# Performance work log

Measured on AMD Instinct MI355X. Metric: run time of the kernel, lower is better.

Reference implementation:

```python
import jax, jax.numpy as jnp
import numpy as np

N_NODES = 50000
N_EDGES = 1600000
D_NODE = 256
D_EDGE = 64
D_MSG = 256          # out_features_msg; each of node/edge halves is D_MSG // 2
D_OUT = 256          # out_features_reduce
H = D_MSG // 2


def setup_inputs() -> dict:
    key = jax.random.key(0)
    ks = jax.random.split(key, 10)
    x = jax.random.normal(ks[0], (N_NODES, D_NODE), dtype=jnp.float32)
    ez = jax.random.normal(ks[1], (N_EDGES, D_EDGE), dtype=jnp.float32)
    src = jax.random.randint(ks[2], (N_EDGES,), 0, N_NODES, dtype=jnp.int32)
    dst = jax.random.randint(ks[3], (N_EDGES,), 0, N_NODES, dtype=jnp.int32)
    Wn = jax.random.normal(ks[4], (H, D_NODE), dtype=jnp.float32) / np.sqrt(D_NODE)
    bn = jax.random.normal(ks[5], (H,), dtype=jnp.float32) * 0.01
    We = jax.random.normal(ks[6], (H, D_EDGE), dtype=jnp.float32) / np.sqrt(D_EDGE)
    be = jax.random.normal(ks[7], (H,), dtype=jnp.float32) * 0.01
    Wr = jax.random.normal(ks[8], (D_OUT, D_MSG), dtype=jnp.float32) / np.sqrt(D_MSG)
    br = jax.random.normal(ks[9], (D_OUT,), dtype=jnp.float32) * 0.01
    return {"x": x, "ez": ez, "src": src, "dst": dst,
            "Wn": Wn, "bn": bn, "We": We, "be": be, "Wr": Wr, "br": br}


def reference(x, ez, src, dst, Wn, bn, We, be, Wr, br):
    n = x.shape[0]
    # node/edge linear projections (message halves)
    hn = x @ Wn.T + bn                 # [N, H]
    he = ez @ We.T + be                # [E, H]
    # message for edge e is concat(hn[src[e]], he[e]); aggregate sums per dst node.
    sum_n = jax.ops.segment_sum(hn[src], dst, num_segments=n)   # [N, H]
    sum_e = jax.ops.segment_sum(he, dst, num_segments=n)        # [N, H]
    deg = jnp.zeros((n,), dtype=x.dtype).at[dst].add(1.0)       # in-degree
    # local self-state: concat(hn, zeros_H); mean over (deg + 1) states.
    denom = (deg + 1.0)[:, None]
    mean_state = jnp.concatenate([(hn + sum_n) / denom, sum_e / denom], axis=-1)  # [N, D_MSG]
    # reduce_layer is affine, so Linear(mean(states)) == mean(Linear(states)).
    out = mean_state @ Wr.T + br       # [N, D_OUT]
    # DGL degree-bucketing: zero-in-degree nodes get zero-filled output.
    out = jnp.where(deg[:, None] > 0, out, jnp.zeros((), dtype=out.dtype))
    return out
```

## Files before the change

kernel.cpp:

```cpp
#include <hip/hip_runtime.h>

#define N_NODES 50000
#define N_EDGES 1600000
#define D_NODE  256
#define D_EDGE  64
#define H       128
#define D_OUT   256

#define NPAD    50176

typedef __attribute__((ext_vector_type(8))) short bf16x8;
typedef __attribute__((ext_vector_type(4))) float f32x4;
typedef __attribute__((ext_vector_type(4))) unsigned short u16x4;

__device__ __forceinline__ float bf2f(unsigned short u) {
    union { unsigned int i; float f; } v; v.i = ((unsigned int)u) << 16; return v.f;
}
__device__ __forceinline__ unsigned short f2bf(float f) {
    union { float f; unsigned int i; } v; v.f = f;
    unsigned int r = v.i + 0x7FFFu + ((v.i >> 16) & 1u);
    return (unsigned short)(r >> 16);
}

__global__ __launch_bounds__(256) void cvt_kernel(
        const float* __restrict__ Wn, const float* __restrict__ We,
        const float* __restrict__ Wr,
        unsigned short* __restrict__ Wn_b, unsigned short* __restrict__ We_b,
        unsigned short* __restrict__ Wr_b) {
    int b = blockIdx.x;
    const float* s; unsigned short* d; int base;
    if (b < 32)      { s = Wn; d = Wn_b; base = b * 1024; }
    else if (b < 40) { s = We; d = We_b; base = (b - 32) * 1024; }
    else             { s = Wr; d = Wr_b; base = (b - 40) * 1024; }
    int i = base + threadIdx.x * 4;
    f32x4 v = *(const f32x4*)(s + i);
    u16x4 o;
    #pragma unroll
    for (int j = 0; j < 4; ++j) o[j] = f2bf(v[j]);
    *(u16x4*)(d + i) = o;
}

__global__ __launch_bounds__(64) void hn_kernel(
        const float* __restrict__ x,
        const unsigned short* __restrict__ Wn_b,
        const float* __restrict__ bn,
        unsigned short* __restrict__ hn) {
    const int lane = threadIdx.x & 63;
    const int m = lane & 15, q = lane >> 4;
    const int n0 = blockIdx.x * 16;

    f32x4 acc[8];
    #pragma unroll
    for (int t = 0; t < 8; ++t)
        #pragma unroll
        for (int r = 0; r < 4; ++r) acc[t][r] = 0.0f;

    const float* xrow = x + (size_t)(n0 + m) * D_NODE + q * 8;
    #pragma unroll
    for (int kk = 0; kk < 8; ++kk) {
        f32x4 a0 = *(const f32x4*)(xrow + kk * 32);
        f32x4 a1 = *(const f32x4*)(xrow + kk * 32 + 4);
        bf16x8 a;
        #pragma unroll
        for (int j = 0; j < 4; ++j) {
            a[j]     = (short)f2bf(a0[j]);
            a[4 + j] = (short)f2bf(a1[j]);
        }
        #pragma unroll
        for (int t = 0; t < 8; ++t) {
            bf16x8 b = *(const bf16x8*)(Wn_b + (size_t)(t * 16 + m) * D_NODE + kk * 32 + q * 8);
            acc[t] = __builtin_amdgcn_mfma_f32_16x16x32_bf16(a, b, acc[t], 0, 0, 0);
        }
    }
    #pragma unroll
    for (int t = 0; t < 8; ++t) {
        int o = t * 16 + m;
        float bv = bn[o];
        #pragma unroll
        for (int r = 0; r < 4; ++r) {
            int node = n0 + q * 4 + r;
            hn[(size_t)node * H + o] = f2bf(acc[t][r] + bv);
        }
    }
}

__global__ __launch_bounds__(256) void hist_kernel(
        const int* __restrict__ dst, unsigned int* __restrict__ cnt) {
    int e = blockIdx.x * 256 + threadIdx.x;
    atomicAdd(&cnt[dst[e]], 1u);
}

__device__ __forceinline__ unsigned int block_scan_incl(unsigned int v, unsigned int* wtot) {
    const int lane = threadIdx.x & 63;
    const int wid = threadIdx.x >> 6;
    unsigned int x = v;
    #pragma unroll
    for (int off = 1; off < 64; off <<= 1) {
        unsigned int y = __shfl_up(x, off, 64);
        if (lane >= off) x += y;
    }
    if (lane == 63) wtot[wid] = x;
    __syncthreads();
    unsigned int wof = 0;
    #pragma unroll
    for (int w = 0; w < 4; ++w) if (w < wid) wof += wtot[w];
    return x + wof;
}

__global__ __launch_bounds__(256) void scan1_kernel(
        const unsigned int* __restrict__ cnt,
        unsigned int* __restrict__ partial,
        unsigned int* __restrict__ blocksum) {
    __shared__ unsigned int wtot[4];
    int i = blockIdx.x * 256 + threadIdx.x;
    unsigned int v = cnt[i];
    unsigned int inc = block_scan_incl(v, wtot);
    partial[i] = inc - v;
    if (threadIdx.x == 255) blocksum[blockIdx.x] = inc;
}

__global__ __launch_bounds__(256) void scan2_kernel(
        const unsigned int* __restrict__ blocksum,
        unsigned int* __restrict__ blockoff) {
    __shared__ unsigned int wtot[4];
    unsigned int v = blocksum[threadIdx.x];
    unsigned int inc = block_scan_incl(v, wtot);
    blockoff[threadIdx.x] = inc - v;
}

__global__ __launch_bounds__(256) void cursor_kernel(
        const unsigned int* __restrict__ partial,
        const unsigned int* __restrict__ blockoff,
        unsigned int* __restrict__ cursor) {
    int i = blockIdx.x * 256 + threadIdx.x;
    cursor[i] = partial[i] + blockoff[blockIdx.x];
}

__global__ __launch_bounds__(256) void scatter_kernel(
        const int* __restrict__ src, const int* __restrict__ dst,
        unsigned int* __restrict__ cursor,
        unsigned long long* __restrict__ eid_src) {
    int e = blockIdx.x * 256 + threadIdx.x;
    int d = dst[e];
    unsigned int s = (unsigned int)src[e];
    unsigned int pos = atomicAdd(&cursor[d], 1u);
    eid_src[pos] = ((unsigned long long)s << 32) | (unsigned int)e;
}

__global__ __launch_bounds__(256) void agg_kernel(
        const unsigned long long* __restrict__ eid_src,
        const unsigned int* __restrict__ cursor,
        const unsigned int* __restrict__ cnt,
        const float* __restrict__ ez,
        const unsigned int* __restrict__ hn32,
        float* __restrict__ sumN, float* __restrict__ sumEZ) {
    const int n = blockIdx.x * 4 + (threadIdx.x >> 6);
    const int lane = threadIdx.x & 63;
    const unsigned int end = cursor[n];
    const unsigned int c = cnt[n];
    const unsigned int beg = end - c;

    float se = 0.0f, sn0 = 0.0f, sn1 = 0.0f;

    for (unsigned int base = beg; base < end; base += 64) {
        int mcnt = (int)(end - base); if (mcnt > 64) mcnt = 64;
        unsigned long long ent = (lane < mcnt) ? eid_src[base + lane] : 0ULL;
        unsigned int elo = (unsigned int)ent;
        unsigned int shi = (unsigned int)(ent >> 32);

        int j = 0;
        for (; j + 4 <= mcnt; j += 4) {
            unsigned int e0 = __shfl(elo, j, 64),     s0i = __shfl(shi, j, 64);
            unsigned int e1 = __shfl(elo, j + 1, 64), s1i = __shfl(shi, j + 1, 64);
            unsigned int e2 = __shfl(elo, j + 2, 64), s2i = __shfl(shi, j + 2, 64);
            unsigned int e3 = __shfl(elo, j + 3, 64), s3i = __shfl(shi, j + 3, 64);
            float a0 = ez[(size_t)e0 * D_EDGE + lane];
            float a1 = ez[(size_t)e1 * D_EDGE + lane];
            float a2 = ez[(size_t)e2 * D_EDGE + lane];
            float a3 = ez[(size_t)e3 * D_EDGE + lane];
            unsigned int h0 = hn32[(size_t)s0i * 64 + lane];
            unsigned int h1 = hn32[(size_t)s1i * 64 + lane];
            unsigned int h2 = hn32[(size_t)s2i * 64 + lane];
            unsigned int h3 = hn32[(size_t)s3i * 64 + lane];
            se += (a0 + a1) + (a2 + a3);
            union { unsigned int u; float f; } lo, hi;
            lo.u = h0 << 16; hi.u = h0 & 0xffff0000u; sn0 += lo.f; sn1 += hi.f;
            lo.u = h1 << 16; hi.u = h1 & 0xffff0000u; sn0 += lo.f; sn1 += hi.f;
            lo.u = h2 << 16; hi.u = h2 & 0xffff0000u; sn0 += lo.f; sn1 += hi.f;
            lo.u = h3 << 16; hi.u = h3 & 0xffff0000u; sn0 += lo.f; sn1 += hi.f;
        }
        for (; j < mcnt; ++j) {
            unsigned int e0 = __shfl(elo, j, 64), s0i = __shfl(shi, j, 64);
            float a0 = ez[(size_t)e0 * D_EDGE + lane];
            unsigned int h0 = hn32[(size_t)s0i * 64 + lane];
            se += a0;
            union { unsigned int u; float f; } lo, hi;
            lo.u = h0 << 16; hi.u = h0 & 0xffff0000u; sn0 += lo.f; sn1 += hi.f;
        }
    }

    sumEZ[(size_t)n * D_EDGE + lane] = se;
    float2 p; p.x = sn0; p.y = sn1;
    *((float2*)(sumN + (size_t)n * H) + lane) = p;
}

__global__ __launch_bounds__(256) void out_kernel(
        const unsigned short* __restrict__ hn,
        const float* __restrict__ sumN,
        const float* __restrict__ sumEZ,
        const unsigned int* __restrict__ deg,
        const unsigned short* __restrict__ We_b,
        const float* __restrict__ be,
        const unsigned short* __restrict__ Wr_b,
        const float* __restrict__ br,
        float* __restrict__ out) {
    __shared__ __align__(16) unsigned short ms[16][264];
    __shared__ float rden[16];
    __shared__ float degf[16];

    const int t = threadIdx.x;
    const int n0 = blockIdx.x * 16;

    if (t < 16) {
        unsigned int dg = deg[n0 + t];
        degf[t] = (float)dg;
        rden[t] = 1.0f / (1.0f + (float)dg);
    }
    __syncthreads();

    {
        int r = t >> 4, c8 = (t & 15) * 8;
        const unsigned short* hp = hn + (size_t)(n0 + r) * H + c8;
        const float* sp = sumN + (size_t)(n0 + r) * H + c8;
        bf16x8 hv = *(const bf16x8*)hp;
        f32x4 s0 = *(const f32x4*)sp;
        f32x4 s1 = *(const f32x4*)(sp + 4);
        float rd = rden[r];
        bf16x8 o;
        #pragma unroll
        for (int j = 0; j < 4; ++j)
            o[j] = (short)f2bf((bf2f((unsigned short)hv[j]) + s0[j]) * rd);
        #pragma unroll
        for (int j = 0; j < 4; ++j)
            o[4 + j] = (short)f2bf((bf2f((unsigned short)hv[4 + j]) + s1[j]) * rd);
        *(bf16x8*)&ms[r][c8] = o;
    }

    {
        const int w = t >> 6, lane = t & 63;
        const int m = lane & 15, q = lane >> 4;
        f32x4 acc[2];
        #pragma unroll
        for (int i = 0; i < 2; ++i)
            #pragma unroll
            for (int r = 0; r < 4; ++r) acc[i][r] = 0.0f;

        #pragma unroll
        for (int kk = 0; kk < 2; ++kk) {
            const float* ap = sumEZ + (size_t)(n0 + m) * D_EDGE + kk * 32 + q * 8;
            f32x4 a0 = *(const f32x4*)ap;
            f32x4 a1 = *(const f32x4*)(ap + 4);
            bf16x8 a;
            #pragma unroll
            for (int j = 0; j < 4; ++j) {
                a[j]     = (short)f2bf(a0[j]);
                a[4 + j] = (short)f2bf(a1[j]);
            }
            #pragma unroll
            for (int i = 0; i < 2; ++i) {
                int o0 = (w + 4 * i) * 16;
                bf16x8 b = *(const bf16x8*)(We_b + (size_t)(o0 + m) * D_EDGE + kk * 32 + q * 8);
                acc[i] = __builtin_amdgcn_mfma_f32_16x16x32_bf16(a, b, acc[i], 0, 0, 0);
            }
        }
        #pragma unroll
        for (int i = 0; i < 2; ++i) {
            int o = (w + 4 * i) * 16 + m;
            float bev = be[o];
            #pragma unroll
            for (int r = 0; r < 4; ++r) {
                int nl = q * 4 + r;
                float val = (acc[i][r] + degf[nl] * bev) * rden[nl];
                ms[nl][128 + o] = f2bf(val);
            }
        }
    }
    __syncthreads();

    {
        const int w = t >> 6, lane = t & 63;
        const int m = lane & 15, q = lane >> 4;
        f32x4 acc[4];
        #pragma unroll
        for (int i = 0; i < 4; ++i)
            #pragma unroll
            for (int r = 0; r < 4; ++r) acc[i][r] = 0.0f;

        #pragma unroll
        for (int kk = 0; kk < 8; ++kk) {
            bf16x8 a = *(const bf16x8*)&ms[m][kk * 32 + q * 8];
            #pragma unroll
            for (int i = 0; i < 4; ++i) {
                int o0 = (w * 4 + i) * 16;
                bf16x8 b = *(const bf16x8*)(Wr_b + (size_t)(o0 + m) * 256 + kk * 32 + q * 8);
                acc[i] = __builtin_amdgcn_mfma_f32_16x16x32_bf16(a, b, acc[i], 0, 0, 0);
            }
        }
        #pragma unroll
        for (int i = 0; i < 4; ++i) {
            int o = (w * 4 + i) * 16 + m;
            float brv = br[o];
            #pragma unroll
            for (int r = 0; r < 4; ++r) {
                int nl = q * 4 + r;
                float val = acc[i][r] + brv;
                if (degf[nl] == 0.0f) val = 0.0f;
                out[(size_t)(n0 + nl) * D_OUT + o] = val;
            }
        }
    }
}

extern "C" void kernel_launch(void* const* d_in, const int* in_sizes, int n_in,
                              void* d_out, int out_size, void* d_ws, size_t ws_size,
                              hipStream_t stream) {
    const float* x  = (const float*)d_in[0];
    const float* ez = (const float*)d_in[1];
    const int* src  = (const int*)d_in[2];
    const int* dst  = (const int*)d_in[3];
    const float* Wn = (const float*)d_in[4];
    const float* bn = (const float*)d_in[5];
    const float* We = (const float*)d_in[6];
    const float* be = (const float*)d_in[7];
    const float* Wr = (const float*)d_in[8];
    const float* br = (const float*)d_in[9];
    float* out      = (float*)d_out;

    unsigned int* cnt      = (unsigned int*)d_ws;
    unsigned int* blocksum = cnt + NPAD;
    unsigned int* blockoff = blocksum + 256;
    unsigned int* partial  = blockoff + 256;
    unsigned int* cursor   = partial + NPAD;
    unsigned long long* eid_src = (unsigned long long*)(cursor + NPAD);
    float* sumN  = (float*)(eid_src + N_EDGES);
    float* sumEZ = sumN + (size_t)N_NODES * H;
    unsigned short* hn = (unsigned short*)(sumEZ + (size_t)N_NODES * D_EDGE);
    unsigned short* Wn_b = hn + (size_t)N_NODES * H;
    unsigned short* We_b = Wn_b + 32768;
    unsigned short* Wr_b = We_b + 8192;

    hipMemsetAsync(d_ws, 0, (size_t)(NPAD + 256) * 4, stream);

    cvt_kernel<<<104, 256, 0, stream>>>(Wn, We, Wr, Wn_b, We_b, Wr_b);
    hn_kernel<<<N_NODES / 16, 64, 0, stream>>>(x, Wn_b, bn, hn);
    hist_kernel<<<N_EDGES / 256, 256, 0, stream>>>(dst, cnt);
    scan1_kernel<<<NPAD / 256, 256, 0, stream>>>(cnt, partial, blocksum);
    scan2_kernel<<<1, 256, 0, stream>>>(blocksum, blockoff);
    cursor_kernel<<<NPAD / 256, 256, 0, stream>>>(partial, blockoff, cursor);
    scatter_kernel<<<N_EDGES / 256, 256, 0, stream>>>(src, dst, cursor, eid_src);
    agg_kernel<<<N_NODES / 4, 256, 0, stream>>>(eid_src, cursor, cnt, ez,
                                                (const unsigned int*)hn, sumN, sumEZ);
    out_kernel<<<N_NODES / 16, 256, 0, stream>>>(hn, sumN, sumEZ, cnt, We_b, be, Wr_b, br, out);
}
```

Measured before the change: 877.8 us.

## Fuse aggregation into output kernel and fold cursor computation into scatter

The per-node aggregation is merged into the output GEMM kernel, so the sums stay in shared memory and the sumN/sumEZ round trip through global memory is gone. The cursor kernel is removed; scatter now adds the block offset to an atomic on the per-block partial prefix. The gather loop is unrolled to 8 edges for more loads in flight, and nontemporal loads and stores are used for streamed data. The cost is that each block handles 16 nodes with 4 nodes per wave done one after another, which lowers the parallelism available to hide gather latency on skewed degrees.

```diff
diff --git a/kernel.cpp b/kernel.cpp
--- a/kernel.cpp
+++ b/kernel.cpp
@@ -58,8 +58,8 @@
     const float* xrow = x + (size_t)(n0 + m) * D_NODE + q * 8;
     #pragma unroll
     for (int kk = 0; kk < 8; ++kk) {
-        f32x4 a0 = *(const f32x4*)(xrow + kk * 32);
-        f32x4 a1 = *(const f32x4*)(xrow + kk * 32 + 4);
+        f32x4 a0 = __builtin_nontemporal_load((const f32x4*)(xrow + kk * 32));
+        f32x4 a1 = __builtin_nontemporal_load((const f32x4*)(xrow + kk * 32 + 4));
         bf16x8 a;
         #pragma unroll
         for (int j = 0; j < 4; ++j) {
@@ -128,126 +128,107 @@
     blockoff[threadIdx.x] = inc - v;
 }
 
-__global__ __launch_bounds__(256) void cursor_kernel(
-        const unsigned int* __restrict__ partial,
-        const unsigned int* __restrict__ blockoff,
-        unsigned int* __restrict__ cursor) {
-    int i = blockIdx.x * 256 + threadIdx.x;
-    cursor[i] = partial[i] + blockoff[blockIdx.x];
-}
-
 __global__ __launch_bounds__(256) void scatter_kernel(
         const int* __restrict__ src, const int* __restrict__ dst,
-        unsigned int* __restrict__ cursor,
+        unsigned int* __restrict__ partial,
+        const unsigned int* __restrict__ blockoff,
         unsigned long long* __restrict__ eid_src) {
     int e = blockIdx.x * 256 + threadIdx.x;
     int d = dst[e];
     unsigned int s = (unsigned int)src[e];
-    unsigned int pos = atomicAdd(&cursor[d], 1u);
+    unsigned int pos = atomicAdd(&partial[d], 1u) + blockoff[d >> 8];
     eid_src[pos] = ((unsigned long long)s << 32) | (unsigned int)e;
 }
 
-__global__ __launch_bounds__(256) void agg_kernel(
+__global__ __launch_bounds__(256) void fused_kernel(
         const unsigned long long* __restrict__ eid_src,
-        const unsigned int* __restrict__ cursor,
+        const unsigned int* __restrict__ partial,
+        const unsigned int* __restrict__ blockoff,
         const unsigned int* __restrict__ cnt,
         const float* __restrict__ ez,
         const unsigned int* __restrict__ hn32,
-        float* __restrict__ sumN, float* __restrict__ sumEZ) {
-    const int n = blockIdx.x * 4 + (threadIdx.x >> 6);
-    const int lane = threadIdx.x & 63;
-    const unsigned int end = cursor[n];
-    const unsigned int c = cnt[n];
-    const unsigned int beg = end - c;
-
-    float se = 0.0f, sn0 = 0.0f, sn1 = 0.0f;
-
-    for (unsigned int base = beg; base < end; base += 64) {
-        int mcnt = (int)(end - base); if (mcnt > 64) mcnt = 64;
-        unsigned long long ent = (lane < mcnt) ? eid_src[base + lane] : 0ULL;
-        unsigned int elo = (unsigned int)ent;
-        unsigned int shi = (unsigned int)(ent >> 32);
-
-        int j = 0;
-        for (; j + 4 <= mcnt; j += 4) {
-            unsigned int e0 = __shfl(elo, j, 64),     s0i = __shfl(shi, j, 64);
-            unsigned int e1 = __shfl(elo, j + 1, 64), s1i = __shfl(shi, j + 1, 64);
-            unsigned int e2 = __shfl(elo, j + 2, 64), s2i = __shfl(shi, j + 2, 64);
-            unsigned int e3 = __shfl(elo, j + 3, 64), s3i = __shfl(shi, j + 3, 64);
-            float a0 = ez[(size_t)e0 * D_EDGE + lane];
-            float a1 = ez[(size_t)e1 * D_EDGE + lane];
-            float a2 = ez[(size_t)e2 * D_EDGE + lane];
-            float a3 = ez[(size_t)e3 * D_EDGE + lane];
-            unsigned int h0 = hn32[(size_t)s0i * 64 + lane];
-            unsigned int h1 = hn32[(size_t)s1i * 64 + lane];
-            unsigned int h2 = hn32[(size_t)s2i * 64 + lane];
-            unsigned int h3 = hn32[(size_t)s3i * 64 + lane];
-            se += (a0 + a1) + (a2 + a3);
-            union { unsigned int u; float f; } lo, hi;
-            lo.u = h0 << 16; hi.u = h0 & 0xffff0000u; sn0 += lo.f; sn1 += hi.f;
-            lo.u = h1 << 16; hi.u = h1 & 0xffff0000u; sn0 += lo.f; sn1 += hi.f;
-            lo.u = h2 << 16; hi.u = h2 & 0xffff0000u; sn0 += lo.f; sn1 += hi.f;
-            lo.u = h3 << 16; hi.u = h3 & 0xffff0000u; sn0 += lo.f; sn1 += hi.f;
-        }
-        for (; j < mcnt; ++j) {
-            unsigned int e0 = __shfl(elo, j, 64), s0i = __shfl(shi, j, 64);
-            float a0 = ez[(size_t)e0 * D_EDGE + lane];
-            unsigned int h0 = hn32[(size_t)s0i * 64 + lane];
-            se += a0;
-            union { unsigned int u; float f; } lo, hi;
-            lo.u = h0 << 16; hi.u = h0 & 0xffff0000u; sn0 += lo.f; sn1 += hi.f;
-        }
-    }
-
-    sumEZ[(size_t)n * D_EDGE + lane] = se;
-    float2 p; p.x = sn0; p.y = sn1;
-    *((float2*)(sumN + (size_t)n * H) + lane) = p;
-}
-
-__global__ __launch_bounds__(256) void out_kernel(
-        const unsigned short* __restrict__ hn,
-        const float* __restrict__ sumN,
-        const float* __restrict__ sumEZ,
-        const unsigned int* __restrict__ deg,
         const unsigned short* __restrict__ We_b,
         const float* __restrict__ be,
         const unsigned short* __restrict__ Wr_b,
         const float* __restrict__ br,
         float* __restrict__ out) {
     __shared__ __align__(16) unsigned short ms[16][264];
+    __shared__ __align__(16) float seL[16][68];
     __shared__ float rden[16];
     __shared__ float degf[16];
 
     const int t = threadIdx.x;
     const int n0 = blockIdx.x * 16;
+    const int wid = t >> 6;
+    const int lane = t & 63;
 
     if (t < 16) {
-        unsigned int dg = deg[n0 + t];
+        unsigned int dg = cnt[n0 + t];
         degf[t] = (float)dg;
         rden[t] = 1.0f / (1.0f + (float)dg);
     }
+
+    for (int nl = 0; nl < 4; ++nl) {
+        const int row = wid * 4 + nl;
+        const int n = n0 + row;
+        const unsigned int c = cnt[n];
+        const unsigned int end = partial[n] + blockoff[n >> 8];
+        const unsigned int beg = end - c;
+        float se = 0.0f, sn0 = 0.0f, sn1 = 0.0f;
+
+        for (unsigned int base = beg; base < end; base += 64) {
+            int mcnt = (int)(end - base); if (mcnt > 64) mcnt = 64;
+            unsigned long long ent = (lane < mcnt)
+                ? __builtin_nontemporal_load(eid_src + base + lane) : 0ULL;
+            unsigned int elo = (unsigned int)ent;
+            unsigned int shi = (unsigned int)(ent >> 32);
+
+            int j = 0;
+            for (; j + 8 <= mcnt; j += 8) {
+                unsigned int e[8], s[8];
+                #pragma unroll
+                for (int u = 0; u < 8; ++u) {
+                    e[u] = __shfl(elo, j + u, 64);
+                    s[u] = __shfl(shi, j + u, 64);
+                }
+                float a[8]; unsigned int h[8];
+                #pragma unroll
+                for (int u = 0; u < 8; ++u)
+                    a[u] = __builtin_nontemporal_load(ez + (size_t)e[u] * D_EDGE + lane);
+                #pragma unroll
+                for (int u = 0; u < 8; ++u)
+                    h[u] = hn32[(size_t)s[u] * 64 + lane];
+                #pragma unroll
+                for (int u = 0; u < 8; ++u) {
+                    se += a[u];
+                    union { unsigned int ui; float f; } lo, hi;
+                    lo.ui = h[u] << 16; hi.ui = h[u] & 0xffff0000u;
+                    sn0 += lo.f; sn1 += hi.f;
+                }
+            }
+            for (; j < mcnt; ++j) {
+                unsigned int e0 = __shfl(elo, j, 64), s0 = __shfl(shi, j, 64);
+                float a0 = __builtin_nontemporal_load(ez + (size_t)e0 * D_EDGE + lane);
+                unsigned int h0 = hn32[(size_t)s0 * 64 + lane];
+                se += a0;
+                union { unsigned int ui; float f; } lo, hi;
+                lo.ui = h0 << 16; hi.ui = h0 & 0xffff0000u;
+                sn0 += lo.f; sn1 += hi.f;
+            }
+        }
+
+        seL[row][lane] = se;
+        unsigned int hv = hn32[(size_t)n * 64 + lane];
+        float rd = 1.0f / (1.0f + (float)c);
+        union { unsigned int ui; float f; } lo, hi;
+        lo.ui = hv << 16; hi.ui = hv & 0xffff0000u;
+        unsigned int p = ((unsigned int)f2bf((hi.f + sn1) * rd) << 16)
+                       |  (unsigned int)f2bf((lo.f + sn0) * rd);
+        *(unsigned int*)&ms[row][2 * lane] = p;
+    }
     __syncthreads();
 
     {
-        int r = t >> 4, c8 = (t & 15) * 8;
-        const unsigned short* hp = hn + (size_t)(n0 + r) * H + c8;
-        const float* sp = sumN + (size_t)(n0 + r) * H + c8;
-        bf16x8 hv = *(const bf16x8*)hp;
-        f32x4 s0 = *(const f32x4*)sp;
-        f32x4 s1 = *(const f32x4*)(sp + 4);
-        float rd = rden[r];
-        bf16x8 o;
-        #pragma unroll
-        for (int j = 0; j < 4; ++j)
-            o[j] = (short)f2bf((bf2f((unsigned short)hv[j]) + s0[j]) * rd);
-        #pragma unroll
-        for (int j = 0; j < 4; ++j)
-            o[4 + j] = (short)f2bf((bf2f((unsigned short)hv[4 + j]) + s1[j]) * rd);
-        *(bf16x8*)&ms[r][c8] = o;
-    }
-
-    {
-        const int w = t >> 6, lane = t & 63;
         const int m = lane & 15, q = lane >> 4;
         f32x4 acc[2];
         #pragma unroll
@@ -257,7 +238,7 @@
 
         #pragma unroll
         for (int kk = 0; kk < 2; ++kk) {
-            const float* ap = sumEZ + (size_t)(n0 + m) * D_EDGE + kk * 32 + q * 8;
+            const float* ap = &seL[m][kk * 32 + q * 8];
             f32x4 a0 = *(const f32x4*)ap;
             f32x4 a1 = *(const f32x4*)(ap + 4);
             bf16x8 a;
@@ -268,14 +249,14 @@
             }
             #pragma unroll
             for (int i = 0; i < 2; ++i) {
-                int o0 = (w + 4 * i) * 16;
+                int o0 = (wid + 4 * i) * 16;
                 bf16x8 b = *(const bf16x8*)(We_b + (size_t)(o0 + m) * D_EDGE + kk * 32 + q * 8);
                 acc[i] = __builtin_amdgcn_mfma_f32_16x16x32_bf16(a, b, acc[i], 0, 0, 0);
             }
         }
         #pragma unroll
         for (int i = 0; i < 2; ++i) {
-            int o = (w + 4 * i) * 16 + m;
+            int o = (wid + 4 * i) * 16 + m;
             float bev = be[o];
             #pragma unroll
             for (int r = 0; r < 4; ++r) {
@@ -288,7 +269,6 @@
     __syncthreads();
 
     {
-        const int w = t >> 6, lane = t & 63;
         const int m = lane & 15, q = lane >> 4;
         f32x4 acc[4];
         #pragma unroll
@@ -301,21 +281,21 @@
             bf16x8 a = *(const bf16x8*)&ms[m][kk * 32 + q * 8];
             #pragma unroll
             for (int i = 0; i < 4; ++i) {
-                int o0 = (w * 4 + i) * 16;
+                int o0 = (wid * 4 + i) * 16;
                 bf16x8 b = *(const bf16x8*)(Wr_b + (size_t)(o0 + m) * 256 + kk * 32 + q * 8);
                 acc[i] = __builtin_amdgcn_mfma_f32_16x16x32_bf16(a, b, acc[i], 0, 0, 0);
             }
         }
         #pragma unroll
         for (int i = 0; i < 4; ++i) {
-            int o = (w * 4 + i) * 16 + m;
+            int o = (wid * 4 + i) * 16 + m;
             float brv = br[o];
             #pragma unroll
             for (int r = 0; r < 4; ++r) {
                 int nl = q * 4 + r;
                 float val = acc[i][r] + brv;
                 if (degf[nl] == 0.0f) val = 0.0f;
-                out[(size_t)(n0 + nl) * D_OUT + o] = val;
+                __builtin_nontemporal_store(val, out + (size_t)(n0 + nl) * D_OUT + o);
             }
         }
     }
@@ -340,11 +320,8 @@
     unsigned int* blocksum = cnt + NPAD;
     unsigned int* blockoff = blocksum + 256;
     unsigned int* partial  = blockoff + 256;
-    unsigned int* cursor   = partial + NPAD;
-    unsigned long long* eid_src = (unsigned long long*)(cursor + NPAD);
-    float* sumN  = (float*)(eid_src + N_EDGES);
-    float* sumEZ = sumN + (size_t)N_NODES * H;
-    unsigned short* hn = (unsigned short*)(sumEZ + (size_t)N_NODES * D_EDGE);
+    unsigned long long* eid_src = (unsigned long long*)(partial + NPAD);
+    unsigned short* hn = (unsigned short*)(eid_src + N_EDGES);
     unsigned short* Wn_b = hn + (size_t)N_NODES * H;
     unsigned short* We_b = Wn_b + 32768;
     unsigned short* Wr_b = We_b + 8192;
@@ -356,9 +333,8 @@
     hist_kernel<<<N_EDGES / 256, 256, 0, stream>>>(dst, cnt);
     scan1_kernel<<<NPAD / 256, 256, 0, stream>>>(cnt, partial, blocksum);
     scan2_kernel<<<1, 256, 0, stream>>>(blocksum, blockoff);
-    cursor_kernel<<<NPAD / 256, 256, 0, stream>>>(partial, blockoff, cursor);
-    scatter_kernel<<<N_EDGES / 256, 256, 0, stream>>>(src, dst, cursor, eid_src);
-    agg_kernel<<<N_NODES / 4, 256, 0, stream>>>(eid_src, cursor, cnt, ez,
-                                                (const unsigned int*)hn, sumN, sumEZ);
-    out_kernel<<<N_NODES / 16, 256, 0, stream>>>(hn, sumN, sumEZ, cnt, We_b, be, Wr_b, br, out);
-}
+    scatter_kernel<<<N_EDGES / 256, 256, 0, stream>>>(src, dst, partial, blockoff, eid_src);
+    fused_kernel<<<N_NODES / 16, 256, 0, stream>>>(eid_src, partial, blockoff, cnt, ez,
+                                                   (const unsigned int*)hn,
+                                                   We_b, be, Wr_b, br, out);
+}
```

Result: no change. 872.6 us (-0.6%).
